# Kernel tuning notes

Measured on AMD Instinct MI355X. Metric: run time of the kernel, lower is better.

## Reference

```python
import jax, jax.numpy as jnp
import numpy as np

IN_F = 512
OUT_F = 256
ALPHA = 0.2  # LeakyReLU negative slope
NEG_INF = -9e15


def setup_inputs() -> dict:
    key = jax.random.key(0)
    k1, k2, k3, k4 = jax.random.split(key, 4)
    N = 8192
    inp = jax.random.normal(k1, (N, IN_F), dtype=jnp.float32)
    adj = jax.random.randint(k2, (N, N), 0, 2, dtype=jnp.int32)
    # xavier_normal with gain=1.414
    std_W = 1.414 * np.sqrt(2.0 / (IN_F + OUT_F))
    W = jax.random.normal(k3, (IN_F, OUT_F), dtype=jnp.float32) * std_W
    std_a = 1.414 * np.sqrt(2.0 / (2 * OUT_F + 1))
    a = jax.random.normal(k4, (2 * OUT_F, 1), dtype=jnp.float32) * std_a
    return {"input": inp, "adj": adj, "W": W, "a": a}


def reference(input, adj, W, a):
    h = input @ W                              # [N, F]
    attn_self = h @ a[:OUT_F]                  # [N, 1]
    attn_neigh = h @ a[OUT_F:]                 # [N, 1]
    dense = attn_self + attn_neigh.T           # [N, N] broadcast add
    dense = jnp.where(dense >= 0, dense, ALPHA * dense)  # leaky relu
    scores = jnp.where(adj > 0, dense, NEG_INF)
    attention = jax.nn.softmax(scores, axis=1)  # dropout p=0.0 -> identity
    h_prime = attention @ h                     # [N, F]
    return jax.nn.elu(h_prime)                  # concat=True branch
```

## Files before the change

kernel.cpp:

```cpp
#include <hip/hip_runtime.h>
#include <hip/hip_bf16.h>
#include <math.h>

#define DEVI static __device__ __forceinline__

using f32x4  = __attribute__((ext_vector_type(4))) float;
using f32x16 = __attribute__((ext_vector_type(16))) float;
using s16x8  = __attribute__((ext_vector_type(8))) short;
using bf16x8 = __attribute__((ext_vector_type(8))) __bf16;
using i32x4  = __attribute__((ext_vector_type(4))) int;
using u32x2  = __attribute__((ext_vector_type(2))) unsigned int;
using u32x4  = __attribute__((ext_vector_type(4))) unsigned int;

constexpr int N   = 8192;
constexpr int KIN = 512;
constexpr int F   = 256;

DEVI unsigned f2bf(float f) {
  unsigned u = __builtin_bit_cast(unsigned, f);
  return ((u + 0x7FFFu + ((u >> 16) & 1u)) >> 16) & 0xFFFFu;
}

DEVI float bfLO(unsigned u) { return __builtin_bit_cast(float, (u & 0xFFFFu) << 16); }
DEVI float bfHI(unsigned u) { return __builtin_bit_cast(float, u & 0xFFFF0000u); }

DEVI unsigned cvtpk(float lo, float hi) {
  unsigned r;
  asm("v_cvt_pk_bf16_f32 %0, %1, %2" : "=v"(r) : "v"(lo), "v"(hi));
  return r;
}

DEVI f32x16 mfma32(s16x8 a, s16x8 b, f32x16 c) {
  return __builtin_amdgcn_mfma_f32_32x32x16_bf16(
      __builtin_bit_cast(bf16x8, a), __builtin_bit_cast(bf16x8, b), c, 0, 0, 0);
}

DEVI void gload16(const void* g, void* lds_uniform) {
  __builtin_amdgcn_global_load_lds(
      (const __attribute__((address_space(1))) unsigned*)g,
      (__attribute__((address_space(3))) unsigned*)lds_uniform, 16, 0, 0);
}

__global__ __launch_bounds__(256) void k_prep_w(const float* __restrict__ W,
                                                unsigned short* __restrict__ Wt) {
  int t = blockIdx.x * 256 + threadIdx.x;
  int c = t >> 6, k0 = (t & 63) * 8;
  s16x8 o;
#pragma unroll
  for (int i = 0; i < 8; ++i) o[i] = (short)f2bf(W[(size_t)(k0 + i) * F + c]);
  *(s16x8*)(Wt + (size_t)c * KIN + k0) = o;
}

__global__ __launch_bounds__(512) void k_gemm1(const float* __restrict__ input,
                                               const unsigned short* __restrict__ Wt,
                                               const float* __restrict__ a_vec,
                                               unsigned short* __restrict__ Ht,
                                               float* __restrict__ E, float* __restrict__ E5,
                                               unsigned* __restrict__ FG) {
  __shared__ __align__(16) char lds[8192 + 32768 + 2048];
  char* ldsA = lds;
  char* ldsW = lds + 8192;
  float* red = (float*)(lds + 8192 + 32768);
  int tid = threadIdx.x, w = tid >> 6, l = tid & 63;
  int r0 = blockIdx.x * 32;
  f32x16 acc;
#pragma unroll
  for (int i = 0; i < 16; ++i) acc[i] = 0.f;

  int lrow8 = l >> 3;
  int koffB = ((l & 7) ^ lrow8) * 8;
  int ra = l & 31, kb = (l >> 5) * 8;
  int colw = w * 32 + ra;

  const int arow = tid >> 4, ac16 = tid & 15;
  const int aoff = (ac16 * 4) ^ ((arow & 7) << 2);
  const float* aR = input + (size_t)(r0 + arow) * KIN + aoff;

  for (int it = 0; it < 8; ++it) {
    int k0 = it * 64;
    __syncthreads();
    gload16(aR + k0, ldsA + w * 1024);
#pragma unroll
    for (int qi = 0; qi < 4; ++qi) {
      int q = 4 * w + qi;
      int c = 8 * q + lrow8;
      gload16(Wt + (size_t)c * KIN + k0 + koffB, ldsW + q * 1024);
    }
    __syncthreads();
    s16x8 av[4], bv[4];
#pragma unroll
    for (int kf = 0; kf < 4; ++kf) {
      int e4 = (kf * 16 + kb) * 4;
      f32x4 a0 = *(const f32x4*)(ldsA + ra * 256 + (e4 ^ ((ra & 7) << 4)));
      f32x4 a1 = *(const f32x4*)(ldsA + ra * 256 + ((e4 + 16) ^ ((ra & 7) << 4)));
      u32x4 ap;
      ap[0] = cvtpk(a0[0], a0[1]); ap[1] = cvtpk(a0[2], a0[3]);
      ap[2] = cvtpk(a1[0], a1[1]); ap[3] = cvtpk(a1[2], a1[3]);
      av[kf] = __builtin_bit_cast(s16x8, ap);
      int kk2 = (kf * 16 + kb) * 2;
      bv[kf] = *(const s16x8*)(ldsW + colw * 128 + (kk2 ^ ((colw & 7) << 4)));
    }
#pragma unroll
    for (int kf = 0; kf < 4; ++kf) acc = mfma32(av[kf], bv[kf], acc);
  }

  float a1v = a_vec[colw], a2v = a_vec[256 + colw];
  int rquad = (l >> 5) * 4;
#pragma unroll
  for (int g = 0; g < 4; ++g) {
    int rowb = g * 8 + rquad;
    unsigned h0 = f2bf(acc[g * 4 + 0]), h1 = f2bf(acc[g * 4 + 1]);
    unsigned h2 = f2bf(acc[g * 4 + 2]), h3 = f2bf(acc[g * 4 + 3]);
    u32x2 pk;
    pk[0] = h0 | (h1 << 16);
    pk[1] = h2 | (h3 << 16);
    *(u32x2*)(Ht + (size_t)colw * N + r0 + rowb) = pk;
  }
#pragma unroll
  for (int g = 0; g < 16; ++g) {
    float vs = acc[g] * a1v;
    float vn = acc[g] * a2v;
#pragma unroll
    for (int m = 1; m <= 16; m <<= 1) {
      vs += __shfl_xor(vs, m, 64);
      vn += __shfl_xor(vn, m, 64);
    }
    if ((l & 31) == 0) {
      int row = (g & 3) + 8 * (g >> 2) + rquad;
      red[row * 8 + w] = vs;
      red[256 + row * 8 + w] = vn;
    }
  }
  __syncthreads();
  if (tid < 32) {
    float s = 0.f, n2 = 0.f;
#pragma unroll
    for (int i = 0; i < 8; ++i) { s += red[tid * 8 + i]; n2 += red[256 + tid * 8 + i]; }
    E[r0 + tid]  = expf(s);
    E5[r0 + tid] = expf(0.2f * s);
    FG[r0 + tid] = f2bf(expf(n2)) | (f2bf(expf(0.2f * n2)) << 16);
  }
}

__global__ __launch_bounds__(512, 4) void k_phase2(const int* __restrict__ adj,
                                                   const unsigned short* __restrict__ Ht,
                                                   const float* __restrict__ E,
                                                   const float* __restrict__ E5,
                                                   const unsigned* __restrict__ FG,
                                                   unsigned short* __restrict__ pacc,
                                                   float* __restrict__ ps) {
  __shared__ __align__(16) char lds[65536 + 8192];
  char* ldsH = lds;
  char* ldsP = lds + 65536;

  const int tid = threadIdx.x, w = tid >> 6, l = tid & 63;
  const int rb = blockIdx.x >> 2, ks = blockIdx.x & 3;
  const int r0 = rb * 64;
  const int jb = ks * 2048;

  const int r = tid >> 3, jc8 = (tid & 7) * 8;
  const float Er = E[r0 + r], E5r = E5[r0 + r];
  float s_part = 0.f;
  const int*      __restrict__ adjR = adj + (size_t)(r0 + r) * N + jb + jc8;
  const unsigned* __restrict__ fgR  = FG + jb + jc8;
  const int pw_byte = r * 128 + ((jc8 * 2) ^ ((r & 7) << 4));

  const int lrow8 = l >> 3;
  const int koffB = ((l & 7) ^ lrow8) * 8;

  const int kh = w >> 2, fgp = (w >> 1) & 1, rg = w & 1;
  const int ra = rg * 32 + (l & 31);
  const int khb = (l >> 5) * 16;
  const int colb = fgp * 128 + (l & 31);
  const int swzA = (ra & 7) << 4;
  const int swzB = (l & 7) << 4;
  const int kt0 = kh * 2;

  f32x16 acc0, acc1, acc2, acc3;
#pragma unroll
  for (int i = 0; i < 16; ++i) { acc0[i] = 0.f; acc1[i] = 0.f; acc2[i] = 0.f; acc3[i] = 0.f; }

#pragma unroll
  for (int qi = 0; qi < 4; ++qi) {
    int q = 4 * w + qi;
    int c = 8 * q + lrow8;
    gload16(Ht + (size_t)c * N + jb + koffB, ldsH + q * 1024);
  }
  i32x4 ad0 = *(const i32x4*)(adjR);
  i32x4 ad1 = *(const i32x4*)(adjR + 4);
  u32x4 fc0 = *(const u32x4*)(fgR);
  u32x4 fc1 = *(const u32x4*)(fgR + 4);

  for (int it = 0; it < 32; ++it) {
    char* Hc = ldsH + (it & 1) * 32768;
    char* Hn = ldsH + ((it & 1) ^ 1) * 32768;
    const int jn = ((it + 1) & 31) * 64;

    {
      float p0 = (ad0[0] != 0) ? fmaxf(Er * bfLO(fc0[0]), E5r * bfHI(fc0[0])) : 0.f;
      float p1 = (ad0[1] != 0) ? fmaxf(Er * bfLO(fc0[1]), E5r * bfHI(fc0[1])) : 0.f;
      float p2 = (ad0[2] != 0) ? fmaxf(Er * bfLO(fc0[2]), E5r * bfHI(fc0[2])) : 0.f;
      float p3 = (ad0[3] != 0) ? fmaxf(Er * bfLO(fc0[3]), E5r * bfHI(fc0[3])) : 0.f;
      float p4 = (ad1[0] != 0) ? fmaxf(Er * bfLO(fc1[0]), E5r * bfHI(fc1[0])) : 0.f;
      float p5 = (ad1[1] != 0) ? fmaxf(Er * bfLO(fc1[1]), E5r * bfHI(fc1[1])) : 0.f;
      float p6 = (ad1[2] != 0) ? fmaxf(Er * bfLO(fc1[2]), E5r * bfHI(fc1[2])) : 0.f;
      float p7 = (ad1[3] != 0) ? fmaxf(Er * bfLO(fc1[3]), E5r * bfHI(fc1[3])) : 0.f;
      s_part += ((p0 + p1) + (p2 + p3)) + ((p4 + p5) + (p6 + p7));
      u32x4 pk;
      pk[0] = cvtpk(p0, p1); pk[1] = cvtpk(p2, p3);
      pk[2] = cvtpk(p4, p5); pk[3] = cvtpk(p6, p7);
      *(u32x4*)(ldsP + pw_byte) = pk;
    }

    ad0 = *(const i32x4*)(adjR + jn);
    ad1 = *(const i32x4*)(adjR + jn + 4);
    fc0 = *(const u32x4*)(fgR + jn);
    fc1 = *(const u32x4*)(fgR + jn + 4);

    asm volatile("s_waitcnt vmcnt(4) lgkmcnt(0)" ::: "memory");
    __builtin_amdgcn_s_barrier();

#pragma unroll
    for (int qi = 0; qi < 4; ++qi) {
      int q = 4 * w + qi;
      int c = 8 * q + lrow8;
      gload16(Ht + (size_t)c * N + jb + jn + koffB, Hn + q * 1024);
    }

#pragma unroll
    for (int t2 = 0; t2 < 2; ++t2) {
      int kk2 = (kt0 + t2) * 32 + khb;
      s16x8 av = *(const s16x8*)(ldsP + ra * 128 + (kk2 ^ swzA));
      s16x8 b0 = *(const s16x8*)(Hc + (colb     ) * 128 + (kk2 ^ swzB));
      s16x8 b1 = *(const s16x8*)(Hc + (colb + 32) * 128 + (kk2 ^ swzB));
      s16x8 b2 = *(const s16x8*)(Hc + (colb + 64) * 128 + (kk2 ^ swzB));
      s16x8 b3 = *(const s16x8*)(Hc + (colb + 96) * 128 + (kk2 ^ swzB));
      acc0 = mfma32(av, b0, acc0);
      acc1 = mfma32(av, b1, acc1);
      acc2 = mfma32(av, b2, acc2);
      acc3 = mfma32(av, b3, acc3);
    }

    asm volatile("s_waitcnt lgkmcnt(0)" ::: "memory");
    __builtin_amdgcn_s_barrier();
  }

  float s = s_part;
#pragma unroll
  for (int m = 1; m <= 4; m <<= 1) s += __shfl_xor(s, m, 64);
  if ((tid & 7) == 0) ps[(size_t)ks * N + r0 + r] = s;

  __syncthreads();
  float* red = (float*)ldsH;
  const int rbase = (fgp * 2 + rg) * 4096;
  if (kh == 1) {
#pragma unroll
    for (int cg = 0; cg < 4; ++cg) {
      const f32x16* a = (cg == 0) ? &acc0 : (cg == 1) ? &acc1 : (cg == 2) ? &acc2 : &acc3;
#pragma unroll
      for (int q = 0; q < 4; ++q) {
        f32x4 v;
#pragma unroll
        for (int i = 0; i < 4; ++i) v[i] = (*a)[q * 4 + i];
        int boff = (cg * 64 + q * 16) ^ ((l & 7) << 4);
        *(f32x4*)((char*)&red[rbase + l * 64] + boff) = v;
      }
    }
  }
  __syncthreads();
  if (kh == 0) {
#pragma unroll
    for (int cg = 0; cg < 4; ++cg) {
      f32x16* a = (cg == 0) ? &acc0 : (cg == 1) ? &acc1 : (cg == 2) ? &acc2 : &acc3;
#pragma unroll
      for (int q = 0; q < 4; ++q) {
        int boff = (cg * 64 + q * 16) ^ ((l & 7) << 4);
        f32x4 v = *(const f32x4*)((const char*)&red[rbase + l * 64] + boff);
#pragma unroll
        for (int i = 0; i < 4; ++i) (*a)[q * 4 + i] += v[i];
      }
    }
    unsigned short* po = pacc + (size_t)ks * N * F;
#pragma unroll
    for (int g = 0; g < 16; ++g) {
      int orow = rg * 32 + (g & 3) + 8 * (g >> 2) + 4 * (l >> 5);
      unsigned short* pr = po + (size_t)(r0 + orow) * F + colb;
      pr[0]  = (unsigned short)f2bf(acc0[g]);
      pr[32] = (unsigned short)f2bf(acc1[g]);
      pr[64] = (unsigned short)f2bf(acc2[g]);
      pr[96] = (unsigned short)f2bf(acc3[g]);
    }
  }
}

__global__ __launch_bounds__(256) void k_combine(const unsigned short* __restrict__ pacc,
                                                 const float* __restrict__ ps,
                                                 float* __restrict__ out) {
  int t = blockIdx.x * 256 + threadIdx.x;
  size_t idx = (size_t)t * 4;
  int row = (int)(idx >> 8);
  f32x4 sum;
#pragma unroll
  for (int i = 0; i < 4; ++i) sum[i] = 0.f;
#pragma unroll
  for (int k = 0; k < 4; ++k) {
    u32x2 q = *(const u32x2*)(pacc + (size_t)k * N * F + idx);
    sum[0] += bfLO(q[0]); sum[1] += bfHI(q[0]);
    sum[2] += bfLO(q[1]); sum[3] += bfHI(q[1]);
  }
  float inv = 1.f / (ps[row] + ps[N + row] + ps[2 * N + row] + ps[3 * N + row]);
  f32x4 o;
#pragma unroll
  for (int i = 0; i < 4; ++i) {
    float v = sum[i] * inv;
    o[i] = v > 0.f ? v : expm1f(v);
  }
  *(f32x4*)(out + idx) = o;
}

extern "C" void kernel_launch(void* const* d_in, const int* in_sizes, int n_in,
                              void* d_out, int out_size, void* d_ws, size_t ws_size,
                              hipStream_t stream) {
  const float* input = (const float*)d_in[0];
  const int*   adj   = (const int*)d_in[1];
  const float* W     = (const float*)d_in[2];
  const float* a     = (const float*)d_in[3];
  float* out = (float*)d_out;
  char* ws = (char*)d_ws;

  unsigned short* pacc = (unsigned short*)(ws);
  unsigned short* Wt   = (unsigned short*)(ws + 8388608);
  unsigned short* Ht   = (unsigned short*)(ws + 16777216);
  float*    E  = (float*)(ws + 20971520);
  float*    E5 = (float*)(ws + 21004288);
  unsigned* FG = (unsigned*)(ws + 21037056);
  float*    ps = (float*)(ws + 21069824);

  hipLaunchKernelGGL(k_prep_w, dim3(64),   dim3(256), 0, stream, W, Wt);
  hipLaunchKernelGGL(k_gemm1,  dim3(256),  dim3(512), 0, stream, input, Wt, a, Ht, E, E5, FG);
  hipLaunchKernelGGL(k_phase2, dim3(512),  dim3(512), 0, stream, adj, Ht, E, E5, FG, pacc, ps);
  hipLaunchKernelGGL(k_combine,dim3(2048), dim3(256), 0, stream, pacc, ps, out);
}
```

Baseline: 112.5 us.

## Store H in MFMA-ready blocked layout and load B fragments directly from global

The first GEMM now writes H in a blocked layout, 16-row j-chunks with feature-major 16-element vectors, so phase2 can load MFMA B operands straight from global/L2 into registers. This removes the 64KB LDS double buffer for H, the global_load_lds staging, and the cross-wave K-split reduction at the end. The warp layout changes so each wave owns 64 columns and the full K range per tile. Each wave now issues its own global loads for H, which raises redundant L2 traffic across waves and blocks, and the loads are not prefetched a tile ahead. LDS use drops to 8KB, and setprio is added around the MFMA bursts.

After: 113.1 us. No clear change (+0.5%).

```diff
diff --git a/kernel.cpp b/kernel.cpp
--- a/kernel.cpp
+++ b/kernel.cpp
@@ -54,7 +54,7 @@
 __global__ __launch_bounds__(512) void k_gemm1(const float* __restrict__ input,
                                                const unsigned short* __restrict__ Wt,
                                                const float* __restrict__ a_vec,
-                                               unsigned short* __restrict__ Ht,
+                                               unsigned short* __restrict__ Hj,
                                                float* __restrict__ E, float* __restrict__ E5,
                                                unsigned* __restrict__ FG) {
   __shared__ __align__(16) char lds[8192 + 32768 + 2048];
@@ -108,13 +108,13 @@
   int rquad = (l >> 5) * 4;
 #pragma unroll
   for (int g = 0; g < 4; ++g) {
-    int rowb = g * 8 + rquad;
+    int jj = r0 + g * 8 + rquad;
     unsigned h0 = f2bf(acc[g * 4 + 0]), h1 = f2bf(acc[g * 4 + 1]);
     unsigned h2 = f2bf(acc[g * 4 + 2]), h3 = f2bf(acc[g * 4 + 3]);
     u32x2 pk;
     pk[0] = h0 | (h1 << 16);
     pk[1] = h2 | (h3 << 16);
-    *(u32x2*)(Ht + (size_t)colw * N + r0 + rowb) = pk;
+    *(u32x2*)(Hj + ((size_t)(jj >> 4)) * 4096 + colw * 16 + (jj & 15)) = pk;
   }
 #pragma unroll
   for (int g = 0; g < 16; ++g) {
@@ -143,15 +143,13 @@
 }
 
 __global__ __launch_bounds__(512, 4) void k_phase2(const int* __restrict__ adj,
-                                                   const unsigned short* __restrict__ Ht,
+                                                   const unsigned short* __restrict__ Hj,
                                                    const float* __restrict__ E,
                                                    const float* __restrict__ E5,
                                                    const unsigned* __restrict__ FG,
                                                    unsigned short* __restrict__ pacc,
                                                    float* __restrict__ ps) {
-  __shared__ __align__(16) char lds[65536 + 8192];
-  char* ldsH = lds;
-  char* ldsP = lds + 65536;
+  __shared__ __align__(16) char ldsP[8192];
 
   const int tid = threadIdx.x, w = tid >> 6, l = tid & 63;
   const int rb = blockIdx.x >> 2, ks = blockIdx.x & 3;
@@ -165,36 +163,36 @@
   const unsigned* __restrict__ fgR  = FG + jb + jc8;
   const int pw_byte = r * 128 + ((jc8 * 2) ^ ((r & 7) << 4));
 
-  const int lrow8 = l >> 3;
-  const int koffB = ((l & 7) ^ lrow8) * 8;
-
-  const int kh = w >> 2, fgp = (w >> 1) & 1, rg = w & 1;
+  const int rg = w & 1, cp = w >> 1;
   const int ra = rg * 32 + (l & 31);
   const int khb = (l >> 5) * 16;
-  const int colb = fgp * 128 + (l & 31);
+  const int colb = cp * 64 + (l & 31);
   const int swzA = (ra & 7) << 4;
-  const int swzB = (l & 7) << 4;
-  const int kt0 = kh * 2;
-
-  f32x16 acc0, acc1, acc2, acc3;
-#pragma unroll
-  for (int i = 0; i < 16; ++i) { acc0[i] = 0.f; acc1[i] = 0.f; acc2[i] = 0.f; acc3[i] = 0.f; }
-
-#pragma unroll
-  for (int qi = 0; qi < 4; ++qi) {
-    int q = 4 * w + qi;
-    int c = 8 * q + lrow8;
-    gload16(Ht + (size_t)c * N + jb + koffB, ldsH + q * 1024);
-  }
+  const int kh8 = (l >> 5) * 8;
+  const unsigned short* __restrict__ HjB =
+      Hj + (size_t)(jb >> 4) * 4096 + colb * 16 + kh8;
+
+  f32x16 acc0, acc1;
+#pragma unroll
+  for (int i = 0; i < 16; ++i) { acc0[i] = 0.f; acc1[i] = 0.f; }
+
   i32x4 ad0 = *(const i32x4*)(adjR);
   i32x4 ad1 = *(const i32x4*)(adjR + 4);
   u32x4 fc0 = *(const u32x4*)(fgR);
   u32x4 fc1 = *(const u32x4*)(fgR + 4);
 
   for (int it = 0; it < 32; ++it) {
-    char* Hc = ldsH + (it & 1) * 32768;
-    char* Hn = ldsH + ((it & 1) ^ 1) * 32768;
     const int jn = ((it + 1) & 31) * 64;
+    const unsigned short* hb = HjB + (size_t)it * 16384;
+
+    s16x8 b00 = *(const s16x8*)(hb);
+    s16x8 b01 = *(const s16x8*)(hb + 512);
+    s16x8 b10 = *(const s16x8*)(hb + 4096);
+    s16x8 b11 = *(const s16x8*)(hb + 4096 + 512);
+    s16x8 b20 = *(const s16x8*)(hb + 8192);
+    s16x8 b21 = *(const s16x8*)(hb + 8192 + 512);
+    s16x8 b30 = *(const s16x8*)(hb + 12288);
+    s16x8 b31 = *(const s16x8*)(hb + 12288 + 512);
 
     {
       float p0 = (ad0[0] != 0) ? fmaxf(Er * bfLO(fc0[0]), E5r * bfHI(fc0[0])) : 0.f;
@@ -217,32 +215,28 @@
     fc0 = *(const u32x4*)(fgR + jn);
     fc1 = *(const u32x4*)(fgR + jn + 4);
 
-    asm volatile("s_waitcnt vmcnt(4) lgkmcnt(0)" ::: "memory");
-    __builtin_amdgcn_s_barrier();
-
-#pragma unroll
-    for (int qi = 0; qi < 4; ++qi) {
-      int q = 4 * w + qi;
-      int c = 8 * q + lrow8;
-      gload16(Ht + (size_t)c * N + jb + jn + koffB, Hn + q * 1024);
-    }
-
-#pragma unroll
-    for (int t2 = 0; t2 < 2; ++t2) {
-      int kk2 = (kt0 + t2) * 32 + khb;
-      s16x8 av = *(const s16x8*)(ldsP + ra * 128 + (kk2 ^ swzA));
-      s16x8 b0 = *(const s16x8*)(Hc + (colb     ) * 128 + (kk2 ^ swzB));
-      s16x8 b1 = *(const s16x8*)(Hc + (colb + 32) * 128 + (kk2 ^ swzB));
-      s16x8 b2 = *(const s16x8*)(Hc + (colb + 64) * 128 + (kk2 ^ swzB));
-      s16x8 b3 = *(const s16x8*)(Hc + (colb + 96) * 128 + (kk2 ^ swzB));
-      acc0 = mfma32(av, b0, acc0);
-      acc1 = mfma32(av, b1, acc1);
-      acc2 = mfma32(av, b2, acc2);
-      acc3 = mfma32(av, b3, acc3);
-    }
-
     asm volatile("s_waitcnt lgkmcnt(0)" ::: "memory");
     __builtin_amdgcn_s_barrier();
+
+    {
+      s16x8 av0 = *(const s16x8*)(ldsP + ra * 128 + ((0 * 32 + khb) ^ swzA));
+      s16x8 av1 = *(const s16x8*)(ldsP + ra * 128 + ((1 * 32 + khb) ^ swzA));
+      s16x8 av2 = *(const s16x8*)(ldsP + ra * 128 + ((2 * 32 + khb) ^ swzA));
+      s16x8 av3 = *(const s16x8*)(ldsP + ra * 128 + ((3 * 32 + khb) ^ swzA));
+      __builtin_amdgcn_s_setprio(1);
+      acc0 = mfma32(av0, b00, acc0);
+      acc1 = mfma32(av0, b01, acc1);
+      acc0 = mfma32(av1, b10, acc0);
+      acc1 = mfma32(av1, b11, acc1);
+      acc0 = mfma32(av2, b20, acc0);
+      acc1 = mfma32(av2, b21, acc1);
+      acc0 = mfma32(av3, b30, acc0);
+      acc1 = mfma32(av3, b31, acc1);
+      __builtin_amdgcn_s_setprio(0);
+    }
+
+    asm volatile("s_waitcnt lgkmcnt(0)" ::: "memory");
+    __builtin_amdgcn_s_barrier();
   }
 
   float s = s_part;
@@ -250,46 +244,13 @@
   for (int m = 1; m <= 4; m <<= 1) s += __shfl_xor(s, m, 64);
   if ((tid & 7) == 0) ps[(size_t)ks * N + r0 + r] = s;
 
-  __syncthreads();
-  float* red = (float*)ldsH;
-  const int rbase = (fgp * 2 + rg) * 4096;
-  if (kh == 1) {
-#pragma unroll
-    for (int cg = 0; cg < 4; ++cg) {
-      const f32x16* a = (cg == 0) ? &acc0 : (cg == 1) ? &acc1 : (cg == 2) ? &acc2 : &acc3;
-#pragma unroll
-      for (int q = 0; q < 4; ++q) {
-        f32x4 v;
-#pragma unroll
-        for (int i = 0; i < 4; ++i) v[i] = (*a)[q * 4 + i];
-        int boff = (cg * 64 + q * 16) ^ ((l & 7) << 4);
-        *(f32x4*)((char*)&red[rbase + l * 64] + boff) = v;
-      }
-    }
-  }
-  __syncthreads();
-  if (kh == 0) {
-#pragma unroll
-    for (int cg = 0; cg < 4; ++cg) {
-      f32x16* a = (cg == 0) ? &acc0 : (cg == 1) ? &acc1 : (cg == 2) ? &acc2 : &acc3;
-#pragma unroll
-      for (int q = 0; q < 4; ++q) {
-        int boff = (cg * 64 + q * 16) ^ ((l & 7) << 4);
-        f32x4 v = *(const f32x4*)((const char*)&red[rbase + l * 64] + boff);
-#pragma unroll
-        for (int i = 0; i < 4; ++i) (*a)[q * 4 + i] += v[i];
-      }
-    }
-    unsigned short* po = pacc + (size_t)ks * N * F;
-#pragma unroll
-    for (int g = 0; g < 16; ++g) {
-      int orow = rg * 32 + (g & 3) + 8 * (g >> 2) + 4 * (l >> 5);
-      unsigned short* pr = po + (size_t)(r0 + orow) * F + colb;
-      pr[0]  = (unsigned short)f2bf(acc0[g]);
-      pr[32] = (unsigned short)f2bf(acc1[g]);
-      pr[64] = (unsigned short)f2bf(acc2[g]);
-      pr[96] = (unsigned short)f2bf(acc3[g]);
-    }
+  unsigned short* po = pacc + (size_t)ks * N * F;
+#pragma unroll
+  for (int g = 0; g < 16; ++g) {
+    int orow = rg * 32 + (g & 3) + 8 * (g >> 2) + 4 * (l >> 5);
+    unsigned short* pr = po + (size_t)(r0 + orow) * F + colb;
+    pr[0]  = (unsigned short)f2bf(acc0[g]);
+    pr[32] = (unsigned short)f2bf(acc1[g]);
   }
 }
 
@@ -330,14 +291,14 @@
 
   unsigned short* pacc = (unsigned short*)(ws);
   unsigned short* Wt   = (unsigned short*)(ws + 8388608);
-  unsigned short* Ht   = (unsigned short*)(ws + 16777216);
+  unsigned short* Hj   = (unsigned short*)(ws + 16777216);
   float*    E  = (float*)(ws + 20971520);
   float*    E5 = (float*)(ws + 21004288);
   unsigned* FG = (unsigned*)(ws + 21037056);
   float*    ps = (float*)(ws + 21069824);
 
   hipLaunchKernelGGL(k_prep_w, dim3(64),   dim3(256), 0, stream, W, Wt);
-  hipLaunchKernelGGL(k_gemm1,  dim3(256),  dim3(512), 0, stream, input, Wt, a, Ht, E, E5, FG);
-  hipLaunchKernelGGL(k_phase2, dim3(512),  dim3(512), 0, stream, adj, Ht, E, E5, FG, pacc, ps);
+  hipLaunchKernelGGL(k_gemm1,  dim3(256),  dim3(512), 0, stream, input, Wt, a, Hj, E, E5, FG);
+  hipLaunchKernelGGL(k_phase2, dim3(512),  dim3(512), 0, stream, adj, Hj, E, E5, FG, pacc, ps);
   hipLaunchKernelGGL(k_combine,dim3(2048), dim3(256), 0, stream, pacc, ps, out);
 }
```
